# Performance work log

Measured on AMD Instinct MI355X. Metric: run time of the kernel, lower is better.

Reference implementation:

```python
import jax, jax.numpy as jnp
import numpy as np

NUM_CATS = 5
EPS = 1e-6


def setup_inputs() -> dict:
    key = jax.random.key(0)
    k1, k2, k3, k4 = jax.random.split(key, 4)
    B, C, H, W = 64, 3, 256, 256
    restored = jax.random.normal(k1, (B, C, H, W), dtype=jnp.float32)
    clean_patch_1 = jax.random.normal(k2, (B, C, H, W), dtype=jnp.float32)
    un = jax.random.uniform(k3, (B, C, H, W), dtype=jnp.float32)
    de_id = jax.random.randint(k4, (B,), 0, NUM_CATS)
    return {"restored": restored, "clean_patch_1": clean_patch_1,
            "de_id": de_id, "un": un}


def _loss(restored, clean, un, de_id):
    B, C, H, W = restored.shape
    E = C * H * W  # elements per sample
    dt = restored.dtype

    onehot = (de_id[:, None] == jnp.arange(NUM_CATS)[None, :])  # [B,5] bool
    m = onehot.astype(dt)                                        # [B,5]
    counts = onehot.sum(0)                                       # [5] int
    nonempty = counts > 0
    safe_counts = jnp.maximum(counts, 1).astype(dt)              # avoid 0-div

    # Per-category mean uncertainty map: un_map[c] = mean_{i: de_id[i]=c} un[i] + eps
    un_sum = jnp.einsum('bk,bchw->kchw', m, un)                  # [5,C,H,W]
    un_map = un_sum / safe_counts[:, None, None, None] + EPS     # [5,C,H,W]
    s = 1.0 / un_map                                             # [5,C,H,W]

    # Per-sample scaled L1 (s gathered by each sample's category)
    absdiff = jnp.abs(clean - restored)                          # [B,C,H,W]
    scaled_sum_per_sample = (absdiff * s[de_id]).sum(axis=(1, 2, 3))  # [B]
    abs_sum_per_sample = absdiff.sum(axis=(1, 2, 3))                  # [B]

    cat_scaled_sum = jnp.einsum('bk,b->k', m, scaled_sum_per_sample)  # [5]
    cat_abs_sum = jnp.einsum('bk,b->k', m, abs_sum_per_sample)        # [5]

    # NOTE: the original code never clears un_hq_list/un_lq_list between
    # categories, so the L1 at category c is the mean over ALL samples from
    # categories 0..c (each scaled by its OWN category's s). Replicate that
    # via cumulative sums/counts over the category axis.
    cum_scaled = jnp.cumsum(cat_scaled_sum)                      # [5]
    cum_elems = jnp.cumsum(counts).astype(dt) * E                # [5]
    cum_l1 = cum_scaled / jnp.maximum(cum_elems, 1.0)            # [5]

    old_loss = jnp.where(nonempty, cat_abs_sum / (safe_counts * E), 0.0)
    un_num = un_map.mean(axis=(1, 2, 3))                         # [5]
    bn = jnp.where(nonempty, 2.0 * jnp.log(un_num), 0.0)
    unc_l1 = jnp.where(nonempty, cum_l1, 0.0)

    cat_losses = unc_l1 + bn                                     # [5]
    num = nonempty.sum().astype(dt)
    total = cat_losses.sum() / num
    return total, cat_losses, old_loss, bn, unc_l1


def reference(restored, clean_patch_1, de_id, un):
    return _loss(restored, clean_patch_1, un, de_id)
```

## Files before the change

kernel.cpp:

```cpp
#include <hip/hip_runtime.h>
#include <math.h>

#define NCAT  5
#define BATCH 64
#define ELEMS 196608
#define POSB  64
#define NBLK  (ELEMS / POSB)
#define TPB   256
#define CHUNK 16
#define GRP   8
#define EPSV  1e-6f

__global__ __launch_bounds__(TPB) void accum_kernel(
    const float* __restrict__ restored,
    const float* __restrict__ clean,
    const int*   __restrict__ de_id,
    const float* __restrict__ un,
    float*       __restrict__ partials)
{
    __shared__ int   sh_de[BATCH];
    __shared__ float sh_inv[NCAT];
    __shared__ float sbuf[2][2 * NCAT][POSB];

    const int tid  = threadIdx.x;
    const int lane = tid & 63;
    const int wave = tid >> 6;

    if (tid < BATCH) {
        int k = de_id[tid];
        sh_de[tid] = k;
        #pragma unroll
        for (int j = 0; j < NCAT; ++j) {
            unsigned long long m = __ballot(k == j);
            if (tid == j) {
                int c = __popcll(m);
                sh_inv[j] = 1.0f / (float)(c > 0 ? c : 1);
            }
        }
    }
    __syncthreads();

    const size_t base = (size_t)(wave * CHUNK) * ELEMS
                      + (size_t)blockIdx.x * POSB + lane;
    const float* rp = restored + base;
    const float* cp = clean + base;
    const float* up = un + base;

    float un_s[NCAT] = {0.f, 0.f, 0.f, 0.f, 0.f};
    float ad_s[NCAT] = {0.f, 0.f, 0.f, 0.f, 0.f};

    float ub[2][GRP], cb[2][GRP], rb[2][GRP];

    #pragma unroll
    for (int i = 0; i < GRP; ++i) {
        const size_t off = (size_t)i * ELEMS;
        ub[0][i] = up[off];
        cb[0][i] = cp[off];
        rb[0][i] = rp[off];
    }

    #pragma unroll
    for (int g = 0; g < CHUNK / GRP; ++g) {
        const int cur = g & 1;
        const int nxt = cur ^ 1;
        if (g < CHUNK / GRP - 1) {
            #pragma unroll
            for (int i = 0; i < GRP; ++i) {
                const size_t off = (size_t)((g + 1) * GRP + i) * ELEMS;
                ub[nxt][i] = up[off];
                cb[nxt][i] = cp[off];
                rb[nxt][i] = rp[off];
            }
        }
        #pragma unroll
        for (int i = 0; i < GRP; ++i) {
            float u  = ub[cur][i];
            float ad = fabsf(cb[cur][i] - rb[cur][i]);
            int   k  = sh_de[wave * CHUNK + g * GRP + i];
            #pragma unroll
            for (int j = 0; j < NCAT; ++j) {
                float m = (k == j) ? 1.0f : 0.0f;
                un_s[j] = fmaf(m, u,  un_s[j]);
                ad_s[j] = fmaf(m, ad, ad_s[j]);
            }
        }
    }

    if (wave >= 2) {
        #pragma unroll
        for (int j = 0; j < NCAT; ++j) {
            sbuf[wave - 2][j][lane]        = un_s[j];
            sbuf[wave - 2][NCAT + j][lane] = ad_s[j];
        }
    }
    __syncthreads();
    if (wave < 2) {
        #pragma unroll
        for (int j = 0; j < NCAT; ++j) {
            un_s[j] += sbuf[wave][j][lane];
            ad_s[j] += sbuf[wave][NCAT + j][lane];
        }
    }
    __syncthreads();
    if (wave == 1) {
        #pragma unroll
        for (int j = 0; j < NCAT; ++j) {
            sbuf[0][j][lane]        = un_s[j];
            sbuf[0][NCAT + j][lane] = ad_s[j];
        }
    }
    __syncthreads();
    if (wave == 0) {
        #pragma unroll
        for (int j = 0; j < NCAT; ++j) {
            un_s[j] += sbuf[0][j][lane];
            ad_s[j] += sbuf[0][NCAT + j][lane];
        }

        float vals[3 * NCAT];
        #pragma unroll
        for (int j = 0; j < NCAT; ++j) {
            float um = fmaf(un_s[j], sh_inv[j], EPSV);
            vals[j]            = ad_s[j] / um;
            vals[NCAT + j]     = ad_s[j];
            vals[2 * NCAT + j] = un_s[j];
        }

        #pragma unroll
        for (int i = 0; i < 3 * NCAT; ++i) {
            float v = vals[i];
            #pragma unroll
            for (int off = 32; off >= 1; off >>= 1)
                v += __shfl_down(v, off, 64);
            vals[i] = v;
        }

        if (lane == 0) {
            #pragma unroll
            for (int i = 0; i < 3 * NCAT; ++i)
                partials[i * NBLK + blockIdx.x] = vals[i];
        }
    }
}

__global__ __launch_bounds__(1024) void epilogue_kernel(
    const int*   __restrict__ de_id,
    const float* __restrict__ partials,
    float*       __restrict__ out)
{
    __shared__ int   sh_cnt[NCAT];
    __shared__ float sh_acc[3 * NCAT];

    const int tid  = threadIdx.x;
    const int lane = tid & 63;
    const int row  = tid >> 6;

    if (tid < 64) {
        int k = de_id[tid];
        #pragma unroll
        for (int j = 0; j < NCAT; ++j) {
            unsigned long long m = __ballot(k == j);
            if (tid == j) sh_cnt[j] = __popcll(m);
        }
    }

    if (row < 3 * NCAT) {
        float v = 0.f;
        #pragma unroll 8
        for (int k = 0; k < NBLK / 64; ++k)
            v += partials[row * NBLK + lane + (k << 6)];
        #pragma unroll
        for (int off = 32; off >= 1; off >>= 1)
            v += __shfl_down(v, off, 64);
        if (lane == 0) sh_acc[row] = v;
    }
    __syncthreads();

    if (tid == 0) {
        const float Ef = (float)ELEMS;
        float cum_s = 0.f;
        long  cum_c = 0;
        float total = 0.f;
        int   num   = 0;

        float cat_losses[NCAT], old_loss[NCAT], bn[NCAT], unc_l1[NCAT];

        for (int j = 0; j < NCAT; ++j) {
            cum_s += sh_acc[j];
            cum_c += sh_cnt[j];
            float cum_elems = (float)cum_c * Ef;
            float cum_l1    = cum_s / fmaxf(cum_elems, 1.0f);

            bool  ne   = sh_cnt[j] > 0;
            float safe = (float)(ne ? sh_cnt[j] : 1);

            old_loss[j]  = ne ? sh_acc[NCAT + j] / (safe * Ef) : 0.f;
            float un_num = sh_acc[2 * NCAT + j] / (safe * Ef) + EPSV;
            bn[j]        = ne ? 2.0f * logf(un_num) : 0.f;
            unc_l1[j]    = ne ? cum_l1 : 0.f;
            cat_losses[j] = unc_l1[j] + bn[j];
            total += cat_losses[j];
            num   += ne ? 1 : 0;
        }
        total /= (float)num;

        out[0] = total;
        for (int j = 0; j < NCAT; ++j) {
            out[1 + j]  = cat_losses[j];
            out[6 + j]  = old_loss[j];
            out[11 + j] = bn[j];
            out[16 + j] = unc_l1[j];
        }
    }
}

extern "C" void kernel_launch(void* const* d_in, const int* in_sizes, int n_in,
                              void* d_out, int out_size, void* d_ws, size_t ws_size,
                              hipStream_t stream) {
    (void)in_sizes; (void)n_in; (void)out_size; (void)ws_size;
    const float* restored = (const float*)d_in[0];
    const float* clean    = (const float*)d_in[1];
    const int*   de_id    = (const int*)d_in[2];
    const float* un       = (const float*)d_in[3];
    float* out      = (float*)d_out;
    float* partials = (float*)d_ws;

    accum_kernel<<<NBLK, TPB, 0, stream>>>(restored, clean, de_id, un, partials);
    epilogue_kernel<<<1, 1024, 0, stream>>>(de_id, partials, out);
}
```

Before: 176.1 us.

## Vectorize accumulation with float4 loads and widen per-block position tile

Each thread now loads float4 from the three input tensors and covers 256 positions per block instead of 64, cutting the block count by four and using 128-bit loads. Per-category accumulators grow to four lanes each, raising register use; launch bounds request 3 blocks per CU and the prefetch group is halved to compensate. The epilogue is reshaped to 16-lane reductions over the smaller partials array with a 256-thread block.

```diff
diff --git a/kernel.cpp b/kernel.cpp
--- a/kernel.cpp
+++ b/kernel.cpp
@@ -4,23 +4,23 @@
 #define NCAT  5
 #define BATCH 64
 #define ELEMS 196608
-#define POSB  64
+#define POSB  256
 #define NBLK  (ELEMS / POSB)
 #define TPB   256
 #define CHUNK 16
-#define GRP   8
+#define GRP   4
 #define EPSV  1e-6f
 
-__global__ __launch_bounds__(TPB) void accum_kernel(
+__global__ __launch_bounds__(TPB, 3) void accum_kernel(
     const float* __restrict__ restored,
     const float* __restrict__ clean,
     const int*   __restrict__ de_id,
     const float* __restrict__ un,
     float*       __restrict__ partials)
 {
-    __shared__ int   sh_de[BATCH];
-    __shared__ float sh_inv[NCAT];
-    __shared__ float sbuf[2][2 * NCAT][POSB];
+    __shared__ int    sh_de[BATCH];
+    __shared__ float  sh_inv[NCAT];
+    __shared__ float4 sbuf[2][2 * NCAT][64];
 
     const int tid  = threadIdx.x;
     const int lane = tid & 63;
@@ -41,19 +41,24 @@
     __syncthreads();
 
     const size_t base = (size_t)(wave * CHUNK) * ELEMS
-                      + (size_t)blockIdx.x * POSB + lane;
-    const float* rp = restored + base;
-    const float* cp = clean + base;
-    const float* up = un + base;
-
-    float un_s[NCAT] = {0.f, 0.f, 0.f, 0.f, 0.f};
-    float ad_s[NCAT] = {0.f, 0.f, 0.f, 0.f, 0.f};
-
-    float ub[2][GRP], cb[2][GRP], rb[2][GRP];
+                      + (size_t)blockIdx.x * POSB + (size_t)lane * 4;
+    const float4* rp = (const float4*)(restored + base);
+    const float4* cp = (const float4*)(clean + base);
+    const float4* up = (const float4*)(un + base);
+    const size_t STR4 = ELEMS / 4;
+
+    float acc_un[NCAT][4];
+    float acc_ad[NCAT][4];
+    #pragma unroll
+    for (int j = 0; j < NCAT; ++j)
+        #pragma unroll
+        for (int ii = 0; ii < 4; ++ii) { acc_un[j][ii] = 0.f; acc_ad[j][ii] = 0.f; }
+
+    float4 ub[2][GRP], cb[2][GRP], rb[2][GRP];
 
     #pragma unroll
     for (int i = 0; i < GRP; ++i) {
-        const size_t off = (size_t)i * ELEMS;
+        const size_t off = (size_t)i * STR4;
         ub[0][i] = up[off];
         cb[0][i] = cp[off];
         rb[0][i] = rp[off];
@@ -66,7 +71,7 @@
         if (g < CHUNK / GRP - 1) {
             #pragma unroll
             for (int i = 0; i < GRP; ++i) {
-                const size_t off = (size_t)((g + 1) * GRP + i) * ELEMS;
+                const size_t off = (size_t)((g + 1) * GRP + i) * STR4;
                 ub[nxt][i] = up[off];
                 cb[nxt][i] = cp[off];
                 rb[nxt][i] = rp[off];
@@ -74,14 +79,25 @@
         }
         #pragma unroll
         for (int i = 0; i < GRP; ++i) {
-            float u  = ub[cur][i];
-            float ad = fabsf(cb[cur][i] - rb[cur][i]);
-            int   k  = sh_de[wave * CHUNK + g * GRP + i];
+            float4 u = ub[cur][i];
+            float4 c = cb[cur][i];
+            float4 r = rb[cur][i];
+            float ad0 = fabsf(c.x - r.x);
+            float ad1 = fabsf(c.y - r.y);
+            float ad2 = fabsf(c.z - r.z);
+            float ad3 = fabsf(c.w - r.w);
+            int   k   = sh_de[wave * CHUNK + g * GRP + i];
             #pragma unroll
             for (int j = 0; j < NCAT; ++j) {
                 float m = (k == j) ? 1.0f : 0.0f;
-                un_s[j] = fmaf(m, u,  un_s[j]);
-                ad_s[j] = fmaf(m, ad, ad_s[j]);
+                acc_un[j][0] = fmaf(m, u.x, acc_un[j][0]);
+                acc_un[j][1] = fmaf(m, u.y, acc_un[j][1]);
+                acc_un[j][2] = fmaf(m, u.z, acc_un[j][2]);
+                acc_un[j][3] = fmaf(m, u.w, acc_un[j][3]);
+                acc_ad[j][0] = fmaf(m, ad0, acc_ad[j][0]);
+                acc_ad[j][1] = fmaf(m, ad1, acc_ad[j][1]);
+                acc_ad[j][2] = fmaf(m, ad2, acc_ad[j][2]);
+                acc_ad[j][3] = fmaf(m, ad3, acc_ad[j][3]);
             }
         }
     }
@@ -89,41 +105,60 @@
     if (wave >= 2) {
         #pragma unroll
         for (int j = 0; j < NCAT; ++j) {
-            sbuf[wave - 2][j][lane]        = un_s[j];
-            sbuf[wave - 2][NCAT + j][lane] = ad_s[j];
+            sbuf[wave - 2][j][lane] =
+                make_float4(acc_un[j][0], acc_un[j][1], acc_un[j][2], acc_un[j][3]);
+            sbuf[wave - 2][NCAT + j][lane] =
+                make_float4(acc_ad[j][0], acc_ad[j][1], acc_ad[j][2], acc_ad[j][3]);
         }
     }
     __syncthreads();
     if (wave < 2) {
         #pragma unroll
         for (int j = 0; j < NCAT; ++j) {
-            un_s[j] += sbuf[wave][j][lane];
-            ad_s[j] += sbuf[wave][NCAT + j][lane];
+            float4 tu = sbuf[wave][j][lane];
+            float4 ta = sbuf[wave][NCAT + j][lane];
+            acc_un[j][0] += tu.x; acc_un[j][1] += tu.y;
+            acc_un[j][2] += tu.z; acc_un[j][3] += tu.w;
+            acc_ad[j][0] += ta.x; acc_ad[j][1] += ta.y;
+            acc_ad[j][2] += ta.z; acc_ad[j][3] += ta.w;
         }
     }
     __syncthreads();
     if (wave == 1) {
         #pragma unroll
         for (int j = 0; j < NCAT; ++j) {
-            sbuf[0][j][lane]        = un_s[j];
-            sbuf[0][NCAT + j][lane] = ad_s[j];
+            sbuf[0][j][lane] =
+                make_float4(acc_un[j][0], acc_un[j][1], acc_un[j][2], acc_un[j][3]);
+            sbuf[0][NCAT + j][lane] =
+                make_float4(acc_ad[j][0], acc_ad[j][1], acc_ad[j][2], acc_ad[j][3]);
         }
     }
     __syncthreads();
     if (wave == 0) {
         #pragma unroll
         for (int j = 0; j < NCAT; ++j) {
-            un_s[j] += sbuf[0][j][lane];
-            ad_s[j] += sbuf[0][NCAT + j][lane];
+            float4 tu = sbuf[0][j][lane];
+            float4 ta = sbuf[0][NCAT + j][lane];
+            acc_un[j][0] += tu.x; acc_un[j][1] += tu.y;
+            acc_un[j][2] += tu.z; acc_un[j][3] += tu.w;
+            acc_ad[j][0] += ta.x; acc_ad[j][1] += ta.y;
+            acc_ad[j][2] += ta.z; acc_ad[j][3] += ta.w;
         }
 
         float vals[3 * NCAT];
         #pragma unroll
         for (int j = 0; j < NCAT; ++j) {
-            float um = fmaf(un_s[j], sh_inv[j], EPSV);
-            vals[j]            = ad_s[j] / um;
-            vals[NCAT + j]     = ad_s[j];
-            vals[2 * NCAT + j] = un_s[j];
+            float s_sc = 0.f, s_ad = 0.f, s_un = 0.f;
+            #pragma unroll
+            for (int ii = 0; ii < 4; ++ii) {
+                float um = fmaf(acc_un[j][ii], sh_inv[j], EPSV);
+                s_sc += acc_ad[j][ii] / um;
+                s_ad += acc_ad[j][ii];
+                s_un += acc_un[j][ii];
+            }
+            vals[j]            = s_sc;
+            vals[NCAT + j]     = s_ad;
+            vals[2 * NCAT + j] = s_un;
         }
 
         #pragma unroll
@@ -143,7 +178,7 @@
     }
 }
 
-__global__ __launch_bounds__(1024) void epilogue_kernel(
+__global__ __launch_bounds__(256) void epilogue_kernel(
     const int*   __restrict__ de_id,
     const float* __restrict__ partials,
     float*       __restrict__ out)
@@ -151,9 +186,7 @@
     __shared__ int   sh_cnt[NCAT];
     __shared__ float sh_acc[3 * NCAT];
 
-    const int tid  = threadIdx.x;
-    const int lane = tid & 63;
-    const int row  = tid >> 6;
+    const int tid = threadIdx.x;
 
     if (tid < 64) {
         int k = de_id[tid];
@@ -164,15 +197,18 @@
         }
     }
 
-    if (row < 3 * NCAT) {
+    if (tid < 240) {
+        const int row    = tid >> 4;
+        const int lane16 = tid & 15;
         float v = 0.f;
-        #pragma unroll 8
-        for (int k = 0; k < NBLK / 64; ++k)
-            v += partials[row * NBLK + lane + (k << 6)];
-        #pragma unroll
-        for (int off = 32; off >= 1; off >>= 1)
-            v += __shfl_down(v, off, 64);
-        if (lane == 0) sh_acc[row] = v;
+        #pragma unroll 4
+        for (int k = 0; k < NBLK / 16; ++k)
+            v += partials[row * NBLK + lane16 + (k << 4)];
+        v += __shfl_down(v, 8, 16);
+        v += __shfl_down(v, 4, 16);
+        v += __shfl_down(v, 2, 16);
+        v += __shfl_down(v, 1, 16);
+        if (lane16 == 0) sh_acc[row] = v;
     }
     __syncthreads();
 
@@ -226,5 +262,5 @@
     float* partials = (float*)d_ws;
 
     accum_kernel<<<NBLK, TPB, 0, stream>>>(restored, clean, de_id, un, partials);
-    epilogue_kernel<<<1, 1024, 0, stream>>>(de_id, partials, out);
+    epilogue_kernel<<<1, 256, 0, stream>>>(de_id, partials, out);
 }
```

Result: no change. 173.6 us (-1.4%).

## Split loss into uncertainty-map pass and vectorized per-sample L1 pass

Applied to the files above, without the earlier changes.

The single fused accumulation kernel becomes two passes. The first pass reads only the uncertainty tensor with float4 loads, builds the per-category inverse mean map s in workspace, and emits per-category sums. The second pass streams clean and restored per sample in contiguous slabs with float4 loads, gathers s by each sample's category, and reduces scaled and plain L1 per block. The epilogue then buckets the per-block partials by category. The aim is wider, more contiguous memory access and more parallelism. The cost is an extra launch and a written-then-reread 4 MB s map.

```diff
diff --git a/kernel.cpp b/kernel.cpp
--- a/kernel.cpp
+++ b/kernel.cpp
@@ -4,23 +4,30 @@
 #define NCAT  5
 #define BATCH 64
 #define ELEMS 196608
-#define POSB  64
-#define NBLK  (ELEMS / POSB)
-#define TPB   256
+#define EPSV  1e-6f
+
+#define POSB  256
+#define NBLK1 (ELEMS / POSB)
 #define CHUNK 16
-#define GRP   8
-#define EPSV  1e-6f
-
-__global__ __launch_bounds__(TPB) void accum_kernel(
-    const float* __restrict__ restored,
-    const float* __restrict__ clean,
+#define GRP   4
+
+#define NSLAB  48
+#define SLABSZ (ELEMS / NSLAB)
+#define NBLK2  (BATCH * NSLAB)
+
+#define WS_S   0
+#define WS_P1  (NCAT * ELEMS)
+#define WS_P2  (WS_P1 + NCAT * NBLK1)
+
+__global__ __launch_bounds__(256) void pass1_kernel(
+    const float* __restrict__ un,
     const int*   __restrict__ de_id,
-    const float* __restrict__ un,
-    float*       __restrict__ partials)
+    float*       __restrict__ s_buf,
+    float*       __restrict__ p1)
 {
-    __shared__ int   sh_de[BATCH];
-    __shared__ float sh_inv[NCAT];
-    __shared__ float sbuf[2][2 * NCAT][POSB];
+    __shared__ int    sh_de[BATCH];
+    __shared__ float  sh_inv[NCAT];
+    __shared__ float4 sbuf[2][NCAT][64];
 
     const int tid  = threadIdx.x;
     const int lane = tid & 63;
@@ -41,23 +48,19 @@
     __syncthreads();
 
     const size_t base = (size_t)(wave * CHUNK) * ELEMS
-                      + (size_t)blockIdx.x * POSB + lane;
-    const float* rp = restored + base;
-    const float* cp = clean + base;
-    const float* up = un + base;
-
-    float un_s[NCAT] = {0.f, 0.f, 0.f, 0.f, 0.f};
-    float ad_s[NCAT] = {0.f, 0.f, 0.f, 0.f, 0.f};
-
-    float ub[2][GRP], cb[2][GRP], rb[2][GRP];
-
-    #pragma unroll
-    for (int i = 0; i < GRP; ++i) {
-        const size_t off = (size_t)i * ELEMS;
-        ub[0][i] = up[off];
-        cb[0][i] = cp[off];
-        rb[0][i] = rp[off];
-    }
+                      + (size_t)blockIdx.x * POSB + (size_t)lane * 4;
+    const float4* up = (const float4*)(un + base);
+    const size_t STR4 = ELEMS / 4;
+
+    float acc_un[NCAT][4];
+    #pragma unroll
+    for (int j = 0; j < NCAT; ++j)
+        #pragma unroll
+        for (int ii = 0; ii < 4; ++ii) acc_un[j][ii] = 0.f;
+
+    float4 ub[2][GRP];
+    #pragma unroll
+    for (int i = 0; i < GRP; ++i) ub[0][i] = up[(size_t)i * STR4];
 
     #pragma unroll
     for (int g = 0; g < CHUNK / GRP; ++g) {
@@ -65,115 +68,183 @@
         const int nxt = cur ^ 1;
         if (g < CHUNK / GRP - 1) {
             #pragma unroll
-            for (int i = 0; i < GRP; ++i) {
-                const size_t off = (size_t)((g + 1) * GRP + i) * ELEMS;
-                ub[nxt][i] = up[off];
-                cb[nxt][i] = cp[off];
-                rb[nxt][i] = rp[off];
-            }
+            for (int i = 0; i < GRP; ++i)
+                ub[nxt][i] = up[(size_t)((g + 1) * GRP + i) * STR4];
         }
         #pragma unroll
         for (int i = 0; i < GRP; ++i) {
-            float u  = ub[cur][i];
-            float ad = fabsf(cb[cur][i] - rb[cur][i]);
-            int   k  = sh_de[wave * CHUNK + g * GRP + i];
+            float4 u = ub[cur][i];
+            int    k = sh_de[wave * CHUNK + g * GRP + i];
             #pragma unroll
             for (int j = 0; j < NCAT; ++j) {
                 float m = (k == j) ? 1.0f : 0.0f;
-                un_s[j] = fmaf(m, u,  un_s[j]);
-                ad_s[j] = fmaf(m, ad, ad_s[j]);
+                acc_un[j][0] = fmaf(m, u.x, acc_un[j][0]);
+                acc_un[j][1] = fmaf(m, u.y, acc_un[j][1]);
+                acc_un[j][2] = fmaf(m, u.z, acc_un[j][2]);
+                acc_un[j][3] = fmaf(m, u.w, acc_un[j][3]);
             }
         }
     }
 
     if (wave >= 2) {
         #pragma unroll
-        for (int j = 0; j < NCAT; ++j) {
-            sbuf[wave - 2][j][lane]        = un_s[j];
-            sbuf[wave - 2][NCAT + j][lane] = ad_s[j];
-        }
+        for (int j = 0; j < NCAT; ++j)
+            sbuf[wave - 2][j][lane] =
+                make_float4(acc_un[j][0], acc_un[j][1], acc_un[j][2], acc_un[j][3]);
     }
     __syncthreads();
     if (wave < 2) {
         #pragma unroll
         for (int j = 0; j < NCAT; ++j) {
-            un_s[j] += sbuf[wave][j][lane];
-            ad_s[j] += sbuf[wave][NCAT + j][lane];
+            float4 t = sbuf[wave][j][lane];
+            acc_un[j][0] += t.x; acc_un[j][1] += t.y;
+            acc_un[j][2] += t.z; acc_un[j][3] += t.w;
         }
     }
     __syncthreads();
     if (wave == 1) {
         #pragma unroll
-        for (int j = 0; j < NCAT; ++j) {
-            sbuf[0][j][lane]        = un_s[j];
-            sbuf[0][NCAT + j][lane] = ad_s[j];
-        }
+        for (int j = 0; j < NCAT; ++j)
+            sbuf[0][j][lane] =
+                make_float4(acc_un[j][0], acc_un[j][1], acc_un[j][2], acc_un[j][3]);
     }
     __syncthreads();
     if (wave == 0) {
-        #pragma unroll
-        for (int j = 0; j < NCAT; ++j) {
-            un_s[j] += sbuf[0][j][lane];
-            ad_s[j] += sbuf[0][NCAT + j][lane];
-        }
-
-        float vals[3 * NCAT];
-        #pragma unroll
-        for (int j = 0; j < NCAT; ++j) {
-            float um = fmaf(un_s[j], sh_inv[j], EPSV);
-            vals[j]            = ad_s[j] / um;
-            vals[NCAT + j]     = ad_s[j];
-            vals[2 * NCAT + j] = un_s[j];
-        }
-
-        #pragma unroll
-        for (int i = 0; i < 3 * NCAT; ++i) {
+        float vals[NCAT];
+        #pragma unroll
+        for (int j = 0; j < NCAT; ++j) {
+            float4 t = sbuf[0][j][lane];
+            acc_un[j][0] += t.x; acc_un[j][1] += t.y;
+            acc_un[j][2] += t.z; acc_un[j][3] += t.w;
+
+            float um0 = fmaf(acc_un[j][0], sh_inv[j], EPSV);
+            float um1 = fmaf(acc_un[j][1], sh_inv[j], EPSV);
+            float um2 = fmaf(acc_un[j][2], sh_inv[j], EPSV);
+            float um3 = fmaf(acc_un[j][3], sh_inv[j], EPSV);
+            float4 sv = make_float4(1.f / um0, 1.f / um1, 1.f / um2, 1.f / um3);
+            *(float4*)(s_buf + (size_t)j * ELEMS
+                       + (size_t)blockIdx.x * POSB + (size_t)lane * 4) = sv;
+
+            vals[j] = acc_un[j][0] + acc_un[j][1] + acc_un[j][2] + acc_un[j][3];
+        }
+
+        #pragma unroll
+        for (int i = 0; i < NCAT; ++i) {
             float v = vals[i];
             #pragma unroll
             for (int off = 32; off >= 1; off >>= 1)
                 v += __shfl_down(v, off, 64);
             vals[i] = v;
         }
-
         if (lane == 0) {
             #pragma unroll
-            for (int i = 0; i < 3 * NCAT; ++i)
-                partials[i * NBLK + blockIdx.x] = vals[i];
-        }
+            for (int i = 0; i < NCAT; ++i)
+                p1[i * NBLK1 + blockIdx.x] = vals[i];
+        }
+    }
+}
+
+__global__ __launch_bounds__(256) void pass2_kernel(
+    const float* __restrict__ restored,
+    const float* __restrict__ clean,
+    const int*   __restrict__ de_id,
+    const float* __restrict__ s_buf,
+    float*       __restrict__ p2)
+{
+    __shared__ float sred[4][2];
+
+    const int tid  = threadIdx.x;
+    const int lane = tid & 63;
+    const int wave = tid >> 6;
+
+    const int b   = blockIdx.x / NSLAB;
+    const int sl  = blockIdx.x % NSLAB;
+    const int cat = de_id[b];
+
+    const size_t pbase = (size_t)sl * SLABSZ + (size_t)wave * (SLABSZ / 4)
+                       + (size_t)lane * 4;
+    const float4* cp = (const float4*)(clean    + (size_t)b   * ELEMS + pbase);
+    const float4* rp = (const float4*)(restored + (size_t)b   * ELEMS + pbase);
+    const float4* sp = (const float4*)(s_buf    + (size_t)cat * ELEMS + pbase);
+
+    float ssum = 0.f, asum = 0.f;
+    #pragma unroll
+    for (int it = 0; it < SLABSZ / 4 / 256; ++it) {
+        float4 c  = cp[it * 64];
+        float4 r  = rp[it * 64];
+        float4 sv = sp[it * 64];
+        float a0 = fabsf(c.x - r.x);
+        float a1 = fabsf(c.y - r.y);
+        float a2 = fabsf(c.z - r.z);
+        float a3 = fabsf(c.w - r.w);
+        asum += (a0 + a1) + (a2 + a3);
+        ssum = fmaf(a0, sv.x, ssum);
+        ssum = fmaf(a1, sv.y, ssum);
+        ssum = fmaf(a2, sv.z, ssum);
+        ssum = fmaf(a3, sv.w, ssum);
+    }
+
+    #pragma unroll
+    for (int off = 32; off >= 1; off >>= 1) {
+        ssum += __shfl_down(ssum, off, 64);
+        asum += __shfl_down(asum, off, 64);
+    }
+    if (lane == 0) { sred[wave][0] = ssum; sred[wave][1] = asum; }
+    __syncthreads();
+    if (tid == 0) {
+        float s = sred[0][0] + sred[1][0] + sred[2][0] + sred[3][0];
+        float a = sred[0][1] + sred[1][1] + sred[2][1] + sred[3][1];
+        p2[blockIdx.x]         = s;
+        p2[NBLK2 + blockIdx.x] = a;
     }
 }
 
 __global__ __launch_bounds__(1024) void epilogue_kernel(
     const int*   __restrict__ de_id,
-    const float* __restrict__ partials,
+    const float* __restrict__ p1,
+    const float* __restrict__ p2,
     float*       __restrict__ out)
 {
     __shared__ int   sh_cnt[NCAT];
+    __shared__ int   sh_cat[BATCH];
     __shared__ float sh_acc[3 * NCAT];
 
     const int tid  = threadIdx.x;
     const int lane = tid & 63;
-    const int row  = tid >> 6;
-
-    if (tid < 64) {
+    const int wave = tid >> 6;
+
+    if (tid < BATCH) {
         int k = de_id[tid];
+        sh_cat[tid] = k;
         #pragma unroll
         for (int j = 0; j < NCAT; ++j) {
             unsigned long long m = __ballot(k == j);
             if (tid == j) sh_cnt[j] = __popcll(m);
         }
     }
-
-    if (row < 3 * NCAT) {
-        float v = 0.f;
-        #pragma unroll 8
-        for (int k = 0; k < NBLK / 64; ++k)
-            v += partials[row * NBLK + lane + (k << 6)];
-        #pragma unroll
-        for (int off = 32; off >= 1; off >>= 1)
-            v += __shfl_down(v, off, 64);
-        if (lane == 0) sh_acc[row] = v;
-    }
+    __syncthreads();
+
+    float v = 0.f;
+    if (wave < 5) {
+        for (int it = 0; it < NBLK2 / 64; ++it) {
+            int col = it * 64 + lane;
+            v += (sh_cat[col / NSLAB] == wave) ? p2[col] : 0.f;
+        }
+    } else if (wave < 10) {
+        const int j = wave - 5;
+        for (int it = 0; it < NBLK2 / 64; ++it) {
+            int col = it * 64 + lane;
+            v += (sh_cat[col / NSLAB] == j) ? p2[NBLK2 + col] : 0.f;
+        }
+    } else if (wave < 15) {
+        const int j = wave - 10;
+        for (int it = 0; it < NBLK1 / 64; ++it)
+            v += p1[j * NBLK1 + it * 64 + lane];
+    }
+    #pragma unroll
+    for (int off = 32; off >= 1; off >>= 1)
+        v += __shfl_down(v, off, 64);
+    if (lane == 0 && wave < 15) sh_acc[wave] = v;
     __syncthreads();
 
     if (tid == 0) {
@@ -222,9 +293,13 @@
     const float* clean    = (const float*)d_in[1];
     const int*   de_id    = (const int*)d_in[2];
     const float* un       = (const float*)d_in[3];
-    float* out      = (float*)d_out;
-    float* partials = (float*)d_ws;
-
-    accum_kernel<<<NBLK, TPB, 0, stream>>>(restored, clean, de_id, un, partials);
-    epilogue_kernel<<<1, 1024, 0, stream>>>(de_id, partials, out);
+    float* out   = (float*)d_out;
+    float* ws    = (float*)d_ws;
+    float* s_buf = ws + WS_S;
+    float* p1    = ws + WS_P1;
+    float* p2    = ws + WS_P2;
+
+    pass1_kernel<<<NBLK1, 256, 0, stream>>>(un, de_id, s_buf, p1);
+    pass2_kernel<<<NBLK2, 256, 0, stream>>>(restored, clean, de_id, s_buf, p2);
+    epilogue_kernel<<<1, 1024, 0, stream>>>(de_id, p1, p2, out);
 }
```

Result: no change. 173.9 us (-1.3%).
